# Kernel optimization log

Measured on AMD Instinct MI355X. Metric: run time of the kernel, lower is better.

## Reference

```python
import jax, jax.numpy as jnp
import numpy as np

B, C, CO, N = 2, 32, 32, 64
MODES, LMAX, RBINS = 16, 2, 16
HALF = MODES // 2
NL = (LMAX + 1) ** 2  # 9 real spherical harmonics up to l=2
M = MODES ** 3
HID = 16  # round(CO * 0.5)


def _build_basis():
    # frequencies of the kept FNO corner modes along each axis
    f = np.concatenate([np.arange(HALF), np.arange(-HALF, 0)]).astype(np.float32)
    kx, ky, kz = np.meshgrid(f, f, f, indexing='ij')
    kx, ky, kz = kx.ravel(), ky.ravel(), kz.ravel()
    r = np.sqrt(kx ** 2 + ky ** 2 + kz ** 2)
    nzm = (r > 0).astype(np.float32)
    inv = np.where(r > 0, 1.0 / np.maximum(r, 1e-9), 0.0)
    ux, uy, uz = kx * inv, ky * inv, kz * inv
    # real spherical harmonics l=0,1,2 (cartesian form); all l>0 vanish at DC
    Y = np.stack([
        0.282095 * np.ones_like(r),
        0.488603 * uy, 0.488603 * uz, 0.488603 * ux,
        1.092548 * ux * uy, 1.092548 * uy * uz,
        0.315392 * (3.0 * uz ** 2 - nzm),
        1.092548 * ux * uz, 0.546274 * (ux ** 2 - uy ** 2)], axis=0)  # [NL, M]
    shell = np.minimum((r / (r.max() + 1e-6) * RBINS).astype(np.int64), RBINS - 1)
    cnt = np.bincount(shell, minlength=RBINS).astype(np.float32)
    w = 1.0 / np.sqrt(np.maximum(cnt, 1.0))
    mask = (shell[None, :] == np.arange(RBINS)[:, None]).astype(np.float32) * w[:, None]  # [RBINS, M]
    return (mask[:, None, :] * Y[None]).reshape(RBINS * NL, M).astype(np.float32)

BASIS = jnp.asarray(_build_basis())  # [K=144, M=4096], fixed projection basis
IDX = jnp.asarray(np.concatenate([np.arange(HALF), np.arange(N - HALF, N)]))  # kept mode indices


def cgelu(z):
    return jax.nn.gelu(z.real) + 1j * jax.nn.gelu(z.imag)


def setup_inputs() -> dict:
    key = jax.random.key(0)
    ks = jax.random.split(key, 17)
    rn = lambda k, s: jax.random.normal(k, s, dtype=jnp.float32)
    return {
        'x': rn(ks[0], (B, C, N, N, N)),
        'w_fno_r': rn(ks[1], (CO, C)) * 0.1, 'w_fno_i': rn(ks[2], (CO, C)) * 0.1,
        'b_fno_r': rn(ks[3], (CO,)) * 0.1, 'b_fno_i': rn(ks[4], (CO,)) * 0.1,
        'w_gate_r': rn(ks[5], (CO,)), 'w_gate_i': rn(ks[6], (CO,)),
        'w_spec_r': rn(ks[7], (RBINS, NL, C, CO)) * 0.1, 'w_spec_i': rn(ks[8], (RBINS, NL, C, CO)) * 0.1,
        'mlp_w1_r': rn(ks[9], (HID, CO)) * 0.1, 'mlp_w1_i': rn(ks[10], (HID, CO)) * 0.1,
        'mlp_b1_r': rn(ks[11], (HID,)) * 0.1, 'mlp_b1_i': rn(ks[12], (HID,)) * 0.1,
        'mlp_w2_r': rn(ks[13], (CO, HID)) * 0.1, 'mlp_w2_i': rn(ks[14], (CO, HID)) * 0.1,
        'mlp_b2_r': rn(ks[15], (CO,)) * 0.1, 'mlp_b2_i': rn(ks[16], (CO,)) * 0.1,
    }


def reference(x, w_fno_r, w_fno_i, b_fno_r, b_fno_i, w_gate_r, w_gate_i,
              w_spec_r, w_spec_i, mlp_w1_r, mlp_w1_i, mlp_b1_r, mlp_b1_i,
              mlp_w2_r, mlp_w2_i, mlp_b2_r, mlp_b2_i):
    cx = lambda r, i: (r + 1j * i).astype(jnp.complex64)
    xc = x.astype(jnp.complex64)
    w_fno, b_fno = cx(w_fno_r, w_fno_i), cx(b_fno_r, b_fno_i)
    w_gate = cx(w_gate_r, w_gate_i)
    w_spec = cx(w_spec_r, w_spec_i)
    w1, b1 = cx(mlp_w1_r, mlp_w1_i), cx(mlp_b1_r, mlp_b1_i)
    w2, b2 = cx(mlp_w2_r, mlp_w2_i), cx(mlp_b2_r, mlp_b2_i)

    # skip paths: complex 1x1-conv ('linear') and complex soft-gating
    skip_fno = jnp.einsum('oc,bcxyz->boxyz', w_fno, xc) + b_fno[None, :, None, None, None]
    skip_mlp = xc * w_gate[None, :, None, None, None]

    # Harmonic layer: FFT -> slice kept modes -> harmonic/radial projection
    # -> complex spectral conv -> inverse projection -> scatter -> iFFT
    xf = jnp.fft.fftn(xc, axes=(-3, -2, -1))
    xs = xf[:, :, IDX[:, None, None], IDX[None, :, None], IDX[None, None, :]].reshape(B, C, M)
    coeffs = jnp.einsum('bcm,km->bck', xs, BASIS).reshape(B, C, RBINS, NL)
    coeffs = jnp.einsum('bisl,slio->bosl', coeffs, w_spec)
    xs2 = jnp.einsum('bck,km->bcm', coeffs.reshape(B, CO, RBINS * NL), BASIS)
    full = jnp.zeros((B, CO, N, N, N), jnp.complex64).at[
        :, :, IDX[:, None, None], IDX[None, :, None], IDX[None, None, :]
    ].set(xs2.reshape(B, CO, MODES, MODES, MODES))
    x_fno = jnp.fft.ifftn(full, axes=(-3, -2, -1))

    x1 = x_fno + skip_fno  # n_layers=1 -> no activation here
    h = cgelu(jnp.einsum('hc,bcxyz->bhxyz', w1, x1) + b1[None, :, None, None, None])
    y = jnp.einsum('oh,bhxyz->boxyz', w2, h) + b2[None, :, None, None, None]
    return (y + skip_mlp).real
```

## Files before the change

kernel.cpp:

```cpp
#include <hip/hip_runtime.h>
#include <hip/hip_bf16.h>

#define PI2 6.283185307179586f

typedef __attribute__((ext_vector_type(8))) short short8;
typedef __attribute__((ext_vector_type(4))) float f32x4;

static const size_t O_Y      = 0;
static const size_t O_W1RT   = 36864;
static const size_t O_W1IT   = 37376;
static const size_t O_W1XR   = 37888;
static const size_t O_W1XI   = 38400;
static const size_t O_B1PR   = 38912;
static const size_t O_B1PI   = 38928;
static const size_t O_WSH    = 38944;
static const size_t O_SHELL  = 38960;
static const size_t O_ORDER  = 43056;
static const size_t O_SSTART = 47152;
static const size_t O_COEF   = 47232;
static const size_t O_COEF2  = 65664;
static const size_t O_XS     = 84096;
static const size_t O_XS2    = 608384;
static const size_t O_T2     = 1132672;
static const size_t O_T1     = 3229824;

static __device__ __forceinline__ float geluf(float v) {
  float u = 0.7978845608028654f * (v + 0.044715f * v * v * v);
  float a = fabsf(u);
  float e = __expf(-2.0f * a);
  float th = (1.0f - e) / (1.0f + e);
  th = copysignf(th, u);
  return 0.5f * v * (1.0f + th);
}

static __device__ __forceinline__ unsigned int f2bfbits(float f) {
  unsigned int u = __float_as_uint(f);
  u += 0x7fffu + ((u >> 16) & 1u);
  return u >> 16;
}

static __device__ __forceinline__ unsigned int pk2(float a, float b) {
  return f2bfbits(a) | (f2bfbits(b) << 16);
}

__global__ __launch_bounds__(256) void k0_init(
    const float* __restrict__ wfr, const float* __restrict__ wfi,
    const float* __restrict__ bfr, const float* __restrict__ bfi,
    const float* __restrict__ w1r, const float* __restrict__ w1i,
    const float* __restrict__ b1r, const float* __restrict__ b1i,
    float* __restrict__ ws) {
  float* Y    = ws + O_Y;
  float* w1rt = ws + O_W1RT;  float* w1it = ws + O_W1IT;
  float* W1xr = ws + O_W1XR;  float* W1xi = ws + O_W1XI;
  float* b1pr = ws + O_B1PR;  float* b1pi = ws + O_B1PI;
  float* wsh  = ws + O_WSH;
  int* shellOf = (int*)(ws + O_SHELL);
  int* order   = (int*)(ws + O_ORDER);
  int* sstart  = (int*)(ws + O_SSTART);

  __shared__ int cnt[16], fill[16], st[17];
  int tid = threadIdx.x;
  if (tid < 16) { cnt[tid] = 0; fill[tid] = 0; }
  __syncthreads();
  for (int m = tid; m < 4096; m += 256) {
    int ix = m >> 8, iy = (m >> 4) & 15, iz = m & 15;
    float kx = (float)(ix < 8 ? ix : ix - 16);
    float ky = (float)(iy < 8 ? iy : iy - 16);
    float kz = (float)(iz < 8 ? iz : iz - 16);
    float r2 = kx*kx + ky*ky + kz*kz;
    float r  = sqrtf(r2);
    float nzm = r2 > 0.f ? 1.f : 0.f;
    float inv = r2 > 0.f ? 1.0f / fmaxf(r, 1e-9f) : 0.f;
    float ux = kx*inv, uy = ky*inv, uz = kz*inv;
    Y[0*4096+m] = 0.282095f;
    Y[1*4096+m] = 0.488603f * uy;
    Y[2*4096+m] = 0.488603f * uz;
    Y[3*4096+m] = 0.488603f * ux;
    Y[4*4096+m] = 1.092548f * ux*uy;
    Y[5*4096+m] = 1.092548f * uy*uz;
    Y[6*4096+m] = 0.315392f * (3.0f*uz*uz - nzm);
    Y[7*4096+m] = 1.092548f * ux*uz;
    Y[8*4096+m] = 0.546274f * (ux*ux - uy*uy);
    float rmax = sqrtf(192.0f);
    float t = r / (rmax + 1e-6f) * 16.0f;
    int sh = (int)t; sh = sh > 15 ? 15 : sh;
    shellOf[m] = sh;
    atomicAdd(&cnt[sh], 1);
  }
  __syncthreads();
  if (tid == 0) { int a = 0; for (int s = 0; s < 16; ++s) { st[s] = a; a += cnt[s]; } st[16] = a; }
  __syncthreads();
  if (tid < 16) wsh[tid] = 1.0f / sqrtf(fmaxf((float)cnt[tid], 1.0f));
  if (tid < 17) sstart[tid] = st[tid];
  for (int m = tid; m < 4096; m += 256) {
    int sh = shellOf[m];
    int p = atomicAdd(&fill[sh], 1);
    order[st[sh] + p] = m;
  }
  for (int e = tid; e < 512; e += 256) {
    int j = e >> 5, c = e & 31;
    float ar = 0.f, ai = 0.f;
    for (int o = 0; o < 32; ++o) {
      float wr_ = w1r[j*32+o], wi_ = w1i[j*32+o];
      float fr  = wfr[o*32+c], fi_ = wfi[o*32+c];
      ar += wr_*fr - wi_*fi_;
      ai += wr_*fi_ + wi_*fr;
    }
    W1xr[c*16+j] = ar;  W1xi[c*16+j] = ai;
    w1rt[c*16+j] = w1r[j*32+c];
    w1it[c*16+j] = w1i[j*32+c];
  }
  if (tid < 16) {
    int j = tid;
    float ar = b1r[j], ai = b1i[j];
    for (int o = 0; o < 32; ++o) {
      ar += w1r[j*32+o]*bfr[o] - w1i[j*32+o]*bfi[o];
      ai += w1r[j*32+o]*bfi[o] + w1i[j*32+o]*bfr[o];
    }
    b1pr[j] = ar; b1pi[j] = ai;
  }
}

__global__ __launch_bounds__(256) void k12_fwd(const float* __restrict__ x, float* __restrict__ T2) {
  __shared__ __align__(16) float zS[4096];
  __shared__ float2 slab[64*17];
  __shared__ float2 tw[16*17];
  float* zP = zS;  float* zQ = zS + 1024;  float* zB = zS + 2048;  float* zD = zS + 3072;
  float* ysum = zS;
  int blk = blockIdx.x;
  const float* src = x + (size_t)blk * 4096;
  int tid = threadIdx.x;

  {
    int y = tid >> 2, zt = tid & 3;
    const float4* s4 = (const float4*)(src + y*64);
    float4 u0 = s4[zt];
    float4 u1 = s4[zt + 4];
    float4 u2 = s4[zt + 8];
    float4 u3 = s4[zt + 12];
    const float* p0 = (const float*)&u0; const float* p1 = (const float*)&u1;
    const float* p2 = (const float*)&u2; const float* p3 = (const float*)&u3;
    int base = 4*zt*64 + y;
    #pragma unroll
    for (int e = 0; e < 4; ++e) {
      float a = p0[e] + p2[e], c = p1[e] + p3[e];
      float bb = p0[e] - p2[e], d = p1[e] - p3[e];
      zP[base + e*64] = a + c;
      zQ[base + e*64] = a - c;
      zB[base + e*64] = bb;
      zD[base + e*64] = d;
    }
  }
  {
    int k = tid >> 4, i2 = tid & 15;
    float f = (float)(k < 8 ? k : k - 16);
    float ang = -PI2 * f * (float)i2 / 64.0f;
    float sw, cw; __sincosf(ang, &sw, &cw);
    tw[k*17 + i2] = make_float2(cw, sw);
  }
  __syncthreads();

  {
    int kz = tid & 15, yq = tid >> 4;
    int j = kz & 3;
    const float2* twp = tw + kz*17;
    float arr[4] = {0.f,0.f,0.f,0.f}, aii[4] = {0.f,0.f,0.f,0.f};
    if ((j & 1) == 0) {
      const float* plane = (j == 0) ? zP : zQ;
      #pragma unroll
      for (int z0 = 0; z0 < 16; ++z0) {
        float2 w = twp[z0];
        float4 s = *(const float4*)&plane[z0*64 + 4*yq];
        arr[0] += s.x*w.x; aii[0] += s.x*w.y;
        arr[1] += s.y*w.x; aii[1] += s.y*w.y;
        arr[2] += s.z*w.x; aii[2] += s.z*w.y;
        arr[3] += s.w*w.x; aii[3] += s.w*w.y;
      }
    } else {
      float dsg = (j == 1) ? -1.f : 1.f;
      #pragma unroll
      for (int z0 = 0; z0 < 16; ++z0) {
        float2 w = twp[z0];
        float4 b = *(const float4*)&zB[z0*64 + 4*yq];
        float4 d = *(const float4*)&zD[z0*64 + 4*yq];
        float swi = dsg * w.y, swr = dsg * w.x;
        arr[0] += b.x*w.x - d.x*swi;  aii[0] += b.x*w.y + d.x*swr;
        arr[1] += b.y*w.x - d.y*swi;  aii[1] += b.y*w.y + d.y*swr;
        arr[2] += b.z*w.x - d.z*swi;  aii[2] += b.z*w.y + d.z*swr;
        arr[3] += b.w*w.x - d.w*swi;  aii[3] += b.w*w.y + d.w*swr;
      }
    }
    int y0 = 4*yq;
    slab[(y0+0)*17 + kz] = make_float2(arr[0], aii[0]);
    slab[(y0+1)*17 + kz] = make_float2(arr[1], aii[1]);
    slab[(y0+2)*17 + kz] = make_float2(arr[2], aii[2]);
    slab[(y0+3)*17 + kz] = make_float2(arr[3], aii[3]);
  }
  __syncthreads();

  {
    int y0 = tid >> 4, kz = tid & 15;
    float2 u0 = slab[(y0     )*17 + kz];
    float2 u1 = slab[(y0 + 16)*17 + kz];
    float2 u2 = slab[(y0 + 32)*17 + kz];
    float2 u3 = slab[(y0 + 48)*17 + kz];
    float Ar = u0.x + u2.x, Ai = u0.y + u2.y;
    float Br = u0.x - u2.x, Bi = u0.y - u2.y;
    float Cr = u1.x + u3.x, Ci = u1.y + u3.y;
    float Dr = u1.x - u3.x, Di = u1.y - u3.y;
    float* yp = ysum + y0*162 + kz*10;
    yp[0] = Ar + Cr;  yp[1] = Ai + Ci;
    yp[2] = Br + Di;  yp[3] = Bi - Dr;
    yp[4] = Ar - Cr;  yp[5] = Ai - Ci;
    yp[6] = Br - Di;  yp[7] = Bi + Dr;
  }
  __syncthreads();

  {
    int kz = tid & 15, kyi = tid >> 4;
    const float* yp = ysum + kz*10 + (kyi & 3)*2;
    const float2* twp = tw + kyi*17;
    float ar = 0.f, ai = 0.f;
    #pragma unroll
    for (int y0 = 0; y0 < 16; ++y0) {
      float sr = yp[y0*162], si = yp[y0*162 + 1];
      float2 w = twp[y0];
      ar += sr*w.x - si*w.y;
      ai += sr*w.y + si*w.x;
    }
    *(float2*)&T2[(size_t)blk*512 + (kyi*16 + kz)*2] = make_float2(ar, ai);
  }
}

__global__ __launch_bounds__(256) void k3_dftx(const float* __restrict__ T2, float* __restrict__ xs) {
  __shared__ float slab[64*34];
  __shared__ float xsum[2592];
  __shared__ float2 twx[16*17];
  int blk = blockIdx.x;
  int bc = blk >> 4, ky = blk & 15;
  int tid = threadIdx.x;
  for (int i = tid; i < 2048; i += 256) {
    int xr = i >> 5, rem = i & 31;
    slab[xr*34 + rem] = T2[((size_t)(bc*64 + xr)*16 + ky)*32 + rem];
  }
  {
    int k = tid >> 4, i2 = tid & 15;
    float f = (float)(k < 8 ? k : k - 16);
    float ang = -PI2 * f * (float)i2 / 64.0f;
    float sw, cw; __sincosf(ang, &sw, &cw);
    twx[k*17 + i2] = make_float2(cw, sw);
  }
  __syncthreads();
  {
    int x0 = tid >> 4, kz = tid & 15;
    const float2* sp = (const float2*)slab;
    float2 u0 = sp[(x0     )*17 + kz];
    float2 u1 = sp[(x0 + 16)*17 + kz];
    float2 u2 = sp[(x0 + 32)*17 + kz];
    float2 u3 = sp[(x0 + 48)*17 + kz];
    float Ar = u0.x + u2.x, Ai = u0.y + u2.y;
    float Br = u0.x - u2.x, Bi = u0.y - u2.y;
    float Cr = u1.x + u3.x, Ci = u1.y + u3.y;
    float Dr = u1.x - u3.x, Di = u1.y - u3.y;
    float* yp = xsum + x0*162 + kz*10;
    yp[0] = Ar + Cr;  yp[1] = Ai + Ci;
    yp[2] = Br + Di;  yp[3] = Bi - Dr;
    yp[4] = Ar - Cr;  yp[5] = Ai - Ci;
    yp[6] = Br - Di;  yp[7] = Bi + Dr;
  }
  __syncthreads();
  {
    int kz = tid & 15, kxi = tid >> 4;
    const float* yp = xsum + kz*10 + (kxi & 3)*2;
    const float2* twp = twx + kxi*17;
    float ar = 0.f, ai = 0.f;
    #pragma unroll
    for (int x0 = 0; x0 < 16; ++x0) {
      float sr = yp[x0*162], si = yp[x0*162 + 1];
      float2 w = twp[x0];
      ar += sr*w.x - si*w.y;
      ai += sr*w.y + si*w.x;
    }
    *(float2*)&xs[(size_t)bc*8192 + (kxi*256 + ky*16 + kz)*2] = make_float2(ar, ai);
  }
}

__global__ __launch_bounds__(256) void k4_proj(const float* __restrict__ xs, const float* __restrict__ Y,
    const int* __restrict__ order, const int* __restrict__ sstart, const float* __restrict__ wsh,
    float* __restrict__ coeffs) {
  int blk = blockIdx.x; int bc = blk >> 4, s = blk & 15;
  int tid = threadIdx.x;
  int st = sstart[s], en = sstart[s+1];
  float ar[9], ai[9];
  #pragma unroll
  for (int l = 0; l < 9; ++l) { ar[l] = 0.f; ai[l] = 0.f; }
  for (int ii = st + tid; ii < en; ii += 256) {
    int m = order[ii];
    float2 v = *(const float2*)&xs[(size_t)bc*8192 + m*2];
    #pragma unroll
    for (int l = 0; l < 9; ++l) {
      float yv = Y[l*4096 + m];
      ar[l] += yv * v.x; ai[l] += yv * v.y;
    }
  }
  #pragma unroll
  for (int l = 0; l < 9; ++l) {
    #pragma unroll
    for (int d = 1; d < 64; d <<= 1) {
      ar[l] += __shfl_xor(ar[l], d, 64);
      ai[l] += __shfl_xor(ai[l], d, 64);
    }
  }
  __shared__ float wred[4][18];
  int wv = tid >> 6, lane = tid & 63;
  if (lane == 0) {
    #pragma unroll
    for (int l = 0; l < 9; ++l) { wred[wv][l] = ar[l]; wred[wv][9 + l] = ai[l]; }
  }
  __syncthreads();
  if (tid < 18) {
    float sum = wred[0][tid] + wred[1][tid] + wred[2][tid] + wred[3][tid];
    float w = wsh[s];
    int l = tid < 9 ? tid : tid - 9;
    int ri = tid < 9 ? 0 : 1;
    coeffs[((size_t)bc*144 + s*9 + l)*2 + ri] = w * sum;
  }
}

__global__ __launch_bounds__(64) void k5_spec(const float* __restrict__ coeffs,
    const float* __restrict__ wsr, const float* __restrict__ wsi, float* __restrict__ coeffs2) {
  int blk = blockIdx.x;
  int b = blk / 144, sl = blk % 144;
  int o = threadIdx.x;
  if (o >= 32) return;
  float ar = 0.f, ai = 0.f;
  for (int i = 0; i < 32; ++i) {
    float cr = coeffs[((size_t)(b*32 + i)*144 + sl)*2];
    float ci = coeffs[((size_t)(b*32 + i)*144 + sl)*2 + 1];
    float wr = wsr[(sl*32 + i)*32 + o];
    float wi = wsi[(sl*32 + i)*32 + o];
    ar += cr*wr - ci*wi;
    ai += cr*wi + ci*wr;
  }
  const float sc = 1.0f / 262144.0f;
  coeffs2[((size_t)(b*32 + o)*144 + sl)*2]     = ar * sc;
  coeffs2[((size_t)(b*32 + o)*144 + sl)*2 + 1] = ai * sc;
}

__global__ __launch_bounds__(256) void k7_unproj(const float* __restrict__ coeffs2, const float* __restrict__ Y,
    const int* __restrict__ shellOf, const float* __restrict__ wsh, float* __restrict__ xs2) {
  int bo = blockIdx.x >> 4;
  int m = ((blockIdx.x & 15) << 8) | threadIdx.x;
  __shared__ float c2[288];
  for (int i = threadIdx.x; i < 288; i += 256) c2[i] = coeffs2[(size_t)bo*288 + i];
  __syncthreads();
  int sh = shellOf[m];
  float w = wsh[sh];
  float ar = 0.f, ai = 0.f;
  #pragma unroll
  for (int l = 0; l < 9; ++l) {
    float yv = Y[l*4096 + m];
    ar += yv * c2[(sh*9 + l)*2];
    ai += yv * c2[(sh*9 + l)*2 + 1];
  }
  xs2[(size_t)bo*8192 + m*2]     = w * ar;
  xs2[(size_t)bo*8192 + m*2 + 1] = w * ai;
}

__global__ __launch_bounds__(256) void k8_invx(const float* __restrict__ xs2, float* __restrict__ U1) {
  __shared__ float slab[512];
  int blk = blockIdx.x;
  int bo = blk >> 4, ky = blk & 15;
  int tid = threadIdx.x;
  for (int i = tid; i < 512; i += 256) {
    int kx = i >> 5, rem = i & 31;
    slab[i] = xs2[(size_t)bo*8192 + kx*512 + ky*32 + rem];
  }
  __syncthreads();
  int kz = tid & 15, grp = tid >> 4;
  float ang = PI2 * (float)grp / 64.0f;
  float sw, cw; __sincosf(ang, &sw, &cw);
  float tr = 1.f, ti = 0.f;
  float sjr[4] = {0.f,0.f,0.f,0.f}, sji[4] = {0.f,0.f,0.f,0.f};
  #pragma unroll
  for (int kx = 0; kx < 16; ++kx) {
    if (kx == 8) ti = -ti;
    float2 v = *(const float2*)&slab[(kx*16 + kz)*2];
    sjr[kx & 3] += v.x*tr - v.y*ti;
    sji[kx & 3] += v.x*ti + v.y*tr;
    float nt = tr*cw - ti*sw; ti = tr*sw + ti*cw; tr = nt;
  }
  float Ar = sjr[0]+sjr[2], Ai = sji[0]+sji[2];
  float Br = sjr[0]-sjr[2], Bi = sji[0]-sji[2];
  float Cr = sjr[1]+sjr[3], Ci = sji[1]+sji[3];
  float Dr = sjr[1]-sjr[3], Di = sji[1]-sji[3];
  *(float2*)&U1[((size_t)(bo*64 + grp     )*16 + ky)*32 + kz*2] = make_float2(Ar+Cr, Ai+Ci);
  *(float2*)&U1[((size_t)(bo*64 + grp + 16)*16 + ky)*32 + kz*2] = make_float2(Br-Di, Bi+Dr);
  *(float2*)&U1[((size_t)(bo*64 + grp + 32)*16 + ky)*32 + kz*2] = make_float2(Ar-Cr, Ai-Ci);
  *(float2*)&U1[((size_t)(bo*64 + grp + 48)*16 + ky)*32 + kz*2] = make_float2(Br+Di, Bi-Dr);
}

__global__ __launch_bounds__(256) void k9_invy(const float* __restrict__ U1, float* __restrict__ U2) {
  __shared__ float slab[512];
  int blk = blockIdx.x;
  int tid = threadIdx.x;
  const float* src = U1 + (size_t)blk * 512;
  for (int i = tid; i < 512; i += 256) slab[i] = src[i];
  __syncthreads();
  int kz = tid & 15, grp = tid >> 4;
  float ang = PI2 * (float)grp / 64.0f;
  float sw, cw; __sincosf(ang, &sw, &cw);
  float tr = 1.f, ti = 0.f;
  float sjr[4] = {0.f,0.f,0.f,0.f}, sji[4] = {0.f,0.f,0.f,0.f};
  #pragma unroll
  for (int ky = 0; ky < 16; ++ky) {
    if (ky == 8) ti = -ti;
    float2 v = *(const float2*)&slab[(ky*16 + kz)*2];
    sjr[ky & 3] += v.x*tr - v.y*ti;
    sji[ky & 3] += v.x*ti + v.y*tr;
    float nt = tr*cw - ti*sw; ti = tr*sw + ti*cw; tr = nt;
  }
  float Ar = sjr[0]+sjr[2], Ai = sji[0]+sji[2];
  float Br = sjr[0]-sjr[2], Bi = sji[0]-sji[2];
  float Cr = sjr[1]+sjr[3], Ci = sji[1]+sji[3];
  float Dr = sjr[1]-sjr[3], Di = sji[1]-sji[3];
  float* dst = U2 + (size_t)blk * 2048;
  *(float2*)&dst[((grp     )*16 + kz)*2] = make_float2(Ar+Cr, Ai+Ci);
  *(float2*)&dst[((grp + 16)*16 + kz)*2] = make_float2(Br-Di, Bi+Dr);
  *(float2*)&dst[((grp + 32)*16 + kz)*2] = make_float2(Ar-Cr, Ai-Ci);
  *(float2*)&dst[((grp + 48)*16 + kz)*2] = make_float2(Br+Di, Bi-Dr);
}

__global__ __launch_bounds__(256) void k10_final(
    const float* __restrict__ x, const float* __restrict__ U2,
    const float* __restrict__ ws,
    const float* __restrict__ w2r, const float* __restrict__ w2i,
    const float* __restrict__ b2r, const float* __restrict__ wgr,
    float* __restrict__ out) {
  const float* w1rt = ws + O_W1RT;  const float* w1it = ws + O_W1IT;
  const float* W1xr = ws + O_W1XR;  const float* W1xi = ws + O_W1XI;
  const float* b1pr = ws + O_B1PR;  const float* b1pi = ws + O_B1PI;

  __shared__ unsigned int xfT[128*33];
  __shared__ __hip_bfloat16 xlT[128*34];
  __shared__ f32x4 hpW4[272];
  unsigned int* hpW = (unsigned int*)hpW4;
  unsigned int* Bt  = (unsigned int*)hpW4;

  int tid = threadIdx.x;
  int blk = blockIdx.x;
  int yb = blk & 31, bx = blk >> 5;
  int b = bx >> 6, xr = bx & 63;
  int y0 = yb * 2;

  int lane = tid & 63, wv = tid >> 6;
  int p = lane & 15, q = lane >> 4;

  union U8 { short8 v; unsigned int u[4]; };

  U8 fAr, fAi;
  {
    int z = wv*16 + p;
    float arj[8], aij[8];
    #pragma unroll
    for (int j = 0; j < 8; ++j) {
      int k = 8*q + j;
      int kz = k & 15;
      float f = (float)(kz < 8 ? kz : kz - 16);
      float s, c; __sincosf(PI2 * f * (float)z / 64.0f, &s, &c);
      arj[j] = (k < 16) ? c : -s;
      aij[j] = (k < 16) ? s : c;
    }
    #pragma unroll
    for (int s2 = 0; s2 < 4; ++s2) {
      fAr.u[s2] = pk2(arj[2*s2], arj[2*s2+1]);
      fAi.u[s2] = pk2(aij[2*s2], aij[2*s2+1]);
    }
  }

  for (int i = tid; i < 1024; i += 256) {
    int ya = i >> 9, c = (i >> 4) & 31, zq = i & 15;
    const float4 v = *(const float4*)&x[(size_t)(b*32 + c)*262144 + (size_t)xr*4096
                                        + (size_t)(y0 + ya)*64 + 4*zq];
    int rb = ((ya << 6) + 4*zq)*34 + c;
    xlT[rb]       = __float2bfloat16(v.x);
    xlT[rb + 34]  = __float2bfloat16(v.y);
    xlT[rb + 68]  = __float2bfloat16(v.z);
    xlT[rb + 102] = __float2bfloat16(v.w);
  }
  {
    int ya = tid >> 7, o = (tid >> 2) & 31, t4 = tid & 3;
    const float4* g4 = (const float4*)(U2 + ((size_t)((b*32 + o)*64 + xr))*2048
                                       + (size_t)(y0 + ya)*32 + 8*t4);
    float4 ga = g4[0], gb = g4[1];
    unsigned int* bp = Bt + (ya*32 + o)*17;
    bp[2*t4]         = pk2(ga.x, ga.z);
    bp[2*t4 + 1]     = pk2(gb.x, gb.z);
    bp[8 + 2*t4]     = pk2(ga.y, ga.w);
    bp[8 + 2*t4 + 1] = pk2(gb.y, gb.w);
  }
  __syncthreads();

  {
    f32x4 zac = {0.f, 0.f, 0.f, 0.f};
    #pragma unroll
    for (int ya = 0; ya < 2; ++ya) {
      #pragma unroll
      for (int ot = 0; ot < 2; ++ot) {
        U8 fB;
        uint4 bv = *(const uint4*)(Bt + (ya*32 + ot*16 + p)*17 + 4*q);
        fB.u[0] = bv.x; fB.u[1] = bv.y; fB.u[2] = bv.z; fB.u[3] = bv.w;
        f32x4 Dr = __builtin_amdgcn_mfma_f32_16x16x32_bf16(fAr.v, fB.v, zac, 0, 0, 0);
        f32x4 Di = __builtin_amdgcn_mfma_f32_16x16x32_bf16(fAi.v, fB.v, zac, 0, 0, 0);
        int rowb = ya*64 + wv*16 + 4*q;
        #pragma unroll
        for (int r = 0; r < 4; ++r)
          xfT[(rowb + r)*33 + ot*16 + p] = pk2(Dr[r], Di[r]);
      }
    }
  }
  __syncthreads();

  {
    int wb = wv * 272;

    U8 fW1r, fW1i, fW1iN, fW1xr, fW1xi, fW2[2];
    #pragma unroll
    for (int s = 0; s < 4; ++s) {
      int c0 = 8*q + 2*s, c1 = c0 + 1;
      fW1r.u[s]  = pk2(w1rt[c0*16 + p], w1rt[c1*16 + p]);
      fW1i.u[s]  = pk2(w1it[c0*16 + p], w1it[c1*16 + p]);
      fW1iN.u[s] = fW1i.u[s] ^ 0x80008000u;
      fW1xr.u[s] = pk2(W1xr[c0*16 + p], W1xr[c1*16 + p]);
      fW1xi.u[s] = pk2(W1xi[c0*16 + p], W1xi[c1*16 + p]);
    }
    #pragma unroll
    for (int mt = 0; mt < 2; ++mt) {
      int o = mt*16 + p;
      #pragma unroll
      for (int s = 0; s < 4; ++s) {
        int k0 = 8*q + 2*s;
        float a  = (k0   < 16) ? w2r[o*16 + k0]      : -w2i[o*16 + k0 - 16];
        float bb = (k0+1 < 16) ? w2r[o*16 + k0 + 1]  : -w2i[o*16 + k0 - 15];
        fW2[mt].u[s] = pk2(a, bb);
      }
    }
    float4 b1r4 = *(const float4*)(b1pr + 4*q);
    float4 b1i4 = *(const float4*)(b1pi + 4*q);
    float b2a[2][4], wga[2][4];
    #pragma unroll
    for (int mt = 0; mt < 2; ++mt) {
      float4 t0 = *(const float4*)(b2r + mt*16 + 4*q);
      float4 t1 = *(const float4*)(wgr + mt*16 + 4*q);
      b2a[mt][0]=t0.x; b2a[mt][1]=t0.y; b2a[mt][2]=t0.z; b2a[mt][3]=t0.w;
      wga[mt][0]=t1.x; wga[mt][1]=t1.y; wga[mt][2]=t1.z; wga[mt][3]=t1.w;
    }
    float b1ra[4] = {b1r4.x, b1r4.y, b1r4.z, b1r4.w};
    float b1ia[4] = {b1i4.x, b1i4.y, b1i4.z, b1i4.w};

    f32x4 zacc = {0.f, 0.f, 0.f, 0.f};
    const unsigned int* xlW = (const unsigned int*)xlT;

    for (int tt = 0; tt < 2; ++tt) {
      int tile = wv*2 + tt;
      int ya = tile >> 2, zg = tile & 3;
      int row = ya*64 + zg*16 + p;

      unsigned int w8[8];
      #pragma unroll
      for (int jj = 0; jj < 8; ++jj) w8[jj] = xfT[row*33 + 8*q + jj];
      U8 FR, FI, XV;
      #pragma unroll
      for (int s = 0; s < 4; ++s) {
        FR.u[s] = __builtin_amdgcn_perm(w8[2*s+1], w8[2*s], 0x05040100u);
        FI.u[s] = __builtin_amdgcn_perm(w8[2*s+1], w8[2*s], 0x07060302u);
        XV.u[s] = xlW[row*17 + 4*q + s];
      }

      f32x4 accR = zacc, accI = zacc;
      accR = __builtin_amdgcn_mfma_f32_16x16x32_bf16(fW1r.v,  FR.v, accR, 0, 0, 0);
      accR = __builtin_amdgcn_mfma_f32_16x16x32_bf16(fW1iN.v, FI.v, accR, 0, 0, 0);
      accR = __builtin_amdgcn_mfma_f32_16x16x32_bf16(fW1xr.v, XV.v, accR, 0, 0, 0);
      accI = __builtin_amdgcn_mfma_f32_16x16x32_bf16(fW1r.v,  FI.v, accI, 0, 0, 0);
      accI = __builtin_amdgcn_mfma_f32_16x16x32_bf16(fW1i.v,  FR.v, accI, 0, 0, 0);
      accI = __builtin_amdgcn_mfma_f32_16x16x32_bf16(fW1xi.v, XV.v, accI, 0, 0, 0);

      float hr_[4], hi_[4];
      #pragma unroll
      for (int r = 0; r < 4; ++r) {
        hr_[r] = geluf(accR[r] + b1ra[r]);
        hi_[r] = geluf(accI[r] + b1ia[r]);
      }
      hpW[wb + 17*p + 2*q]     = pk2(hr_[0], hr_[1]);
      hpW[wb + 17*p + 2*q + 1] = pk2(hr_[2], hr_[3]);
      hpW[wb + 17*p + 8 + 2*q]     = pk2(hi_[0], hi_[1]);
      hpW[wb + 17*p + 8 + 2*q + 1] = pk2(hi_[2], hi_[3]);

      U8 FH;
      #pragma unroll
      for (int s = 0; s < 4; ++s) FH.u[s] = hpW[wb + 17*p + 4*q + s];

      #pragma unroll
      for (int mt = 0; mt < 2; ++mt) {
        f32x4 accO = __builtin_amdgcn_mfma_f32_16x16x32_bf16(fW2[mt].v, FH.v, zacc, 0, 0, 0);
        #pragma unroll
        for (int r = 0; r < 4; ++r) {
          int o = mt*16 + q*4 + r;
          int z = zg*16 + p;
          float xv = __bfloat162float(xlT[row*34 + o]);
          out[(size_t)(b*32 + o)*262144 + (size_t)xr*4096 + (size_t)(y0 + ya)*64 + z]
              = accO[r] + b2a[mt][r] + wga[mt][r]*xv;
        }
      }
    }
  }
}

extern "C" void kernel_launch(void* const* d_in, const int* in_sizes, int n_in,
                              void* d_out, int out_size, void* d_ws, size_t ws_size,
                              hipStream_t stream) {
  (void)in_sizes; (void)n_in; (void)out_size; (void)ws_size;
  const float* x   = (const float*)d_in[0];
  const float* wfr = (const float*)d_in[1];
  const float* wfi = (const float*)d_in[2];
  const float* bfr = (const float*)d_in[3];
  const float* bfi = (const float*)d_in[4];
  const float* wgr = (const float*)d_in[5];
  const float* wsr = (const float*)d_in[7];
  const float* wsi = (const float*)d_in[8];
  const float* w1r = (const float*)d_in[9];
  const float* w1i = (const float*)d_in[10];
  const float* b1r = (const float*)d_in[11];
  const float* b1i = (const float*)d_in[12];
  const float* w2r = (const float*)d_in[13];
  const float* w2i = (const float*)d_in[14];
  const float* b2r = (const float*)d_in[15];
  float* out = (float*)d_out;
  float* ws  = (float*)d_ws;

  float* T1      = ws + O_T1;
  float* T2      = ws + O_T2;
  float* xs      = ws + O_XS;
  float* xs2     = ws + O_XS2;
  float* coeffs  = ws + O_COEF;
  float* coeffs2 = ws + O_COEF2;
  float* Y       = ws + O_Y;
  int* shellOf   = (int*)(ws + O_SHELL);
  int* order     = (int*)(ws + O_ORDER);
  int* sstart    = (int*)(ws + O_SSTART);
  float* wsh     = ws + O_WSH;

  hipLaunchKernelGGL(k0_init,  dim3(1),    dim3(256), 0, stream, wfr, wfi, bfr, bfi, w1r, w1i, b1r, b1i, ws);
  hipLaunchKernelGGL(k12_fwd,  dim3(4096), dim3(256), 0, stream, x, T2);
  hipLaunchKernelGGL(k3_dftx,  dim3(1024), dim3(256), 0, stream, T2, xs);
  hipLaunchKernelGGL(k4_proj,  dim3(1024), dim3(256), 0, stream, xs, Y, order, sstart, wsh, coeffs);
  hipLaunchKernelGGL(k5_spec,  dim3(288),  dim3(64),  0, stream, coeffs, wsr, wsi, coeffs2);
  hipLaunchKernelGGL(k7_unproj,dim3(1024), dim3(256), 0, stream, coeffs2, Y, shellOf, wsh, xs2);
  hipLaunchKernelGGL(k8_invx,  dim3(1024), dim3(256), 0, stream, xs2, T2);
  hipLaunchKernelGGL(k9_invy,  dim3(4096), dim3(256), 0, stream, T2, T1);
  hipLaunchKernelGGL(k10_final,dim3(4096), dim3(256), 0, stream, x, T1, ws, w2r, w2i, b2r, wgr, out);
}
```

Measured before the change: 265.2 us.

## Fuse spectral conv, unprojection and inverse x-DFT; use bf16 MFMA for inverse y-DFT

Merges the spectral-weight contraction, the inverse harmonic projection and the inverse x-axis DFT into one kernel. Each block now recomputes the 144 spectral coefficients it needs for its (b,o) pair, using a transposed copy of the spectral weights built by a new prep kernel, so the coeffs2 and xs2 round trips through global memory go away. The inverse y-DFT is rewritten as a pair of 16x16x32 bf16 MFMA matmuls with twiddle factors computed in registers, replacing the scalar twiddle-recurrence loop. In exchange, the spectral contraction is repeated 16 times per (b,o) and the y-DFT drops to bf16 precision.

```diff
diff --git a/kernel.cpp b/kernel.cpp
--- a/kernel.cpp
+++ b/kernel.cpp
@@ -18,9 +18,8 @@
 static const size_t O_ORDER  = 43056;
 static const size_t O_SSTART = 47152;
 static const size_t O_COEF   = 47232;
-static const size_t O_COEF2  = 65664;
 static const size_t O_XS     = 84096;
-static const size_t O_XS2    = 608384;
+static const size_t O_WST    = 608384;
 static const size_t O_T2     = 1132672;
 static const size_t O_T1     = 3229824;
 
@@ -121,6 +120,17 @@
   }
 }
 
+__global__ __launch_bounds__(256) void k0b_wst(const float* __restrict__ wsr,
+    const float* __restrict__ wsi, float* __restrict__ ws) {
+  float* wst = ws + O_WST;
+  int o = blockIdx.x;
+  for (int e = threadIdx.x; e < 4608; e += 256) {
+    int i = e / 144, sl = e - i*144;
+    wst[(size_t)o*9216 + i*288 + sl*2]     = wsr[(sl*32 + i)*32 + o];
+    wst[(size_t)o*9216 + i*288 + sl*2 + 1] = wsi[(sl*32 + i)*32 + o];
+  }
+}
+
 __global__ __launch_bounds__(256) void k12_fwd(const float* __restrict__ x, float* __restrict__ T2) {
   __shared__ __align__(16) float zS[4096];
   __shared__ float2 slab[64*17];
@@ -327,56 +337,54 @@
   }
 }
 
-__global__ __launch_bounds__(64) void k5_spec(const float* __restrict__ coeffs,
-    const float* __restrict__ wsr, const float* __restrict__ wsi, float* __restrict__ coeffs2) {
-  int blk = blockIdx.x;
-  int b = blk / 144, sl = blk % 144;
-  int o = threadIdx.x;
-  if (o >= 32) return;
-  float ar = 0.f, ai = 0.f;
-  for (int i = 0; i < 32; ++i) {
-    float cr = coeffs[((size_t)(b*32 + i)*144 + sl)*2];
-    float ci = coeffs[((size_t)(b*32 + i)*144 + sl)*2 + 1];
-    float wr = wsr[(sl*32 + i)*32 + o];
-    float wi = wsi[(sl*32 + i)*32 + o];
-    ar += cr*wr - ci*wi;
-    ai += cr*wi + ci*wr;
-  }
-  const float sc = 1.0f / 262144.0f;
-  coeffs2[((size_t)(b*32 + o)*144 + sl)*2]     = ar * sc;
-  coeffs2[((size_t)(b*32 + o)*144 + sl)*2 + 1] = ai * sc;
-}
-
-__global__ __launch_bounds__(256) void k7_unproj(const float* __restrict__ coeffs2, const float* __restrict__ Y,
-    const int* __restrict__ shellOf, const float* __restrict__ wsh, float* __restrict__ xs2) {
-  int bo = blockIdx.x >> 4;
-  int m = ((blockIdx.x & 15) << 8) | threadIdx.x;
+__global__ __launch_bounds__(256) void k857(const float* __restrict__ coeffs,
+    const float* __restrict__ ws, float* __restrict__ U1) {
+  const float* wst = ws + O_WST;
+  const float* Y   = ws + O_Y;
+  const int* shellOf = (const int*)(ws + O_SHELL);
+  const float* wsh = ws + O_WSH;
   __shared__ float c2[288];
-  for (int i = threadIdx.x; i < 288; i += 256) c2[i] = coeffs2[(size_t)bo*288 + i];
-  __syncthreads();
-  int sh = shellOf[m];
-  float w = wsh[sh];
-  float ar = 0.f, ai = 0.f;
-  #pragma unroll
-  for (int l = 0; l < 9; ++l) {
-    float yv = Y[l*4096 + m];
-    ar += yv * c2[(sh*9 + l)*2];
-    ai += yv * c2[(sh*9 + l)*2 + 1];
-  }
-  xs2[(size_t)bo*8192 + m*2]     = w * ar;
-  xs2[(size_t)bo*8192 + m*2 + 1] = w * ai;
-}
-
-__global__ __launch_bounds__(256) void k8_invx(const float* __restrict__ xs2, float* __restrict__ U1) {
   __shared__ float slab[512];
   int blk = blockIdx.x;
   int bo = blk >> 4, ky = blk & 15;
+  int b = bo >> 5, o = bo & 31;
   int tid = threadIdx.x;
-  for (int i = tid; i < 512; i += 256) {
-    int kx = i >> 5, rem = i & 31;
-    slab[i] = xs2[(size_t)bo*8192 + kx*512 + ky*32 + rem];
-  }
-  __syncthreads();
+
+  if (tid < 144) {
+    int sl = tid;
+    const float* cp = coeffs + ((size_t)b*4608 + sl)*2;
+    const float* wp = wst + (size_t)o*9216 + sl*2;
+    float ar = 0.f, ai = 0.f;
+    #pragma unroll 4
+    for (int i = 0; i < 32; ++i) {
+      float cr = cp[i*288], ci = cp[i*288 + 1];
+      float wr = wp[i*288], wi = wp[i*288 + 1];
+      ar += cr*wr - ci*wi;
+      ai += cr*wi + ci*wr;
+    }
+    const float sc = 1.0f / 262144.0f;
+    c2[sl*2]     = ar * sc;
+    c2[sl*2 + 1] = ai * sc;
+  }
+  __syncthreads();
+
+  {
+    int kxi = tid >> 4, kz = tid & 15;
+    int m = kxi*256 + ky*16 + kz;
+    int sh = shellOf[m];
+    float w = wsh[sh];
+    float ar = 0.f, ai = 0.f;
+    #pragma unroll
+    for (int l = 0; l < 9; ++l) {
+      float yv = Y[l*4096 + m];
+      ar += yv * c2[(sh*9 + l)*2];
+      ai += yv * c2[(sh*9 + l)*2 + 1];
+    }
+    slab[tid*2]     = w * ar;
+    slab[tid*2 + 1] = w * ai;
+  }
+  __syncthreads();
+
   int kz = tid & 15, grp = tid >> 4;
   float ang = PI2 * (float)grp / 64.0f;
   float sw, cw; __sincosf(ang, &sw, &cw);
@@ -401,34 +409,64 @@
 }
 
 __global__ __launch_bounds__(256) void k9_invy(const float* __restrict__ U1, float* __restrict__ U2) {
-  __shared__ float slab[512];
+  __shared__ unsigned int Bt[16*17];
   int blk = blockIdx.x;
   int tid = threadIdx.x;
-  const float* src = U1 + (size_t)blk * 512;
-  for (int i = tid; i < 512; i += 256) slab[i] = src[i];
-  __syncthreads();
-  int kz = tid & 15, grp = tid >> 4;
-  float ang = PI2 * (float)grp / 64.0f;
-  float sw, cw; __sincosf(ang, &sw, &cw);
-  float tr = 1.f, ti = 0.f;
-  float sjr[4] = {0.f,0.f,0.f,0.f}, sji[4] = {0.f,0.f,0.f,0.f};
-  #pragma unroll
-  for (int ky = 0; ky < 16; ++ky) {
-    if (ky == 8) ti = -ti;
-    float2 v = *(const float2*)&slab[(ky*16 + kz)*2];
-    sjr[ky & 3] += v.x*tr - v.y*ti;
-    sji[ky & 3] += v.x*ti + v.y*tr;
-    float nt = tr*cw - ti*sw; ti = tr*sw + ti*cw; tr = nt;
-  }
-  float Ar = sjr[0]+sjr[2], Ai = sji[0]+sji[2];
-  float Br = sjr[0]-sjr[2], Bi = sji[0]-sji[2];
-  float Cr = sjr[1]+sjr[3], Ci = sji[1]+sji[3];
-  float Dr = sjr[1]-sjr[3], Di = sji[1]-sji[3];
-  float* dst = U2 + (size_t)blk * 2048;
-  *(float2*)&dst[((grp     )*16 + kz)*2] = make_float2(Ar+Cr, Ai+Ci);
-  *(float2*)&dst[((grp + 16)*16 + kz)*2] = make_float2(Br-Di, Bi+Dr);
-  *(float2*)&dst[((grp + 32)*16 + kz)*2] = make_float2(Ar-Cr, Ai-Ci);
-  *(float2*)&dst[((grp + 48)*16 + kz)*2] = make_float2(Br+Di, Bi-Dr);
+  int lane = tid & 63, wv = tid >> 6;
+  int p = lane & 15, q = lane >> 4;
+
+  union U8 { short8 v; unsigned int u[4]; };
+
+  U8 fAr, fAi;
+  {
+    int y = wv*16 + p;
+    float arj[8], aij[8];
+    #pragma unroll
+    for (int j = 0; j < 8; ++j) {
+      int k = 8*q + j;
+      int ky = k & 15;
+      float f = (float)(ky < 8 ? ky : ky - 16);
+      float s, c; __sincosf(PI2 * f * (float)y / 64.0f, &s, &c);
+      arj[j] = (k < 16) ? c : -s;
+      aij[j] = (k < 16) ? s : c;
+    }
+    #pragma unroll
+    for (int s2 = 0; s2 < 4; ++s2) {
+      fAr.u[s2] = pk2(arj[2*s2], arj[2*s2+1]);
+      fAi.u[s2] = pk2(aij[2*s2], aij[2*s2+1]);
+    }
+  }
+
+  {
+    int kz = tid >> 4, w = tid & 15;
+    const float* u = U1 + (size_t)blk * 512;
+    if (w < 8) {
+      float a = u[(2*w    )*32 + kz*2];
+      float b = u[(2*w + 1)*32 + kz*2];
+      Bt[kz*17 + w] = pk2(a, b);
+    } else {
+      int w2 = w - 8;
+      float a = u[(2*w2    )*32 + kz*2 + 1];
+      float b = u[(2*w2 + 1)*32 + kz*2 + 1];
+      Bt[kz*17 + w] = pk2(a, b);
+    }
+  }
+  __syncthreads();
+
+  {
+    U8 fB;
+    uint4 bv = *(const uint4*)(Bt + p*17 + 4*q);
+    fB.u[0] = bv.x; fB.u[1] = bv.y; fB.u[2] = bv.z; fB.u[3] = bv.w;
+    f32x4 zac = {0.f, 0.f, 0.f, 0.f};
+    f32x4 Dr = __builtin_amdgcn_mfma_f32_16x16x32_bf16(fAr.v, fB.v, zac, 0, 0, 0);
+    f32x4 Di = __builtin_amdgcn_mfma_f32_16x16x32_bf16(fAi.v, fB.v, zac, 0, 0, 0);
+    float2* dst = (float2*)(U2 + (size_t)blk * 2048);
+    #pragma unroll
+    for (int r = 0; r < 4; ++r) {
+      int y = wv*16 + 4*q + r;
+      dst[y*16 + p] = make_float2(Dr[r], Di[r]);
+    }
+  }
 }
 
 __global__ __launch_bounds__(256) void k10_final(
@@ -641,22 +679,18 @@
   float* T1      = ws + O_T1;
   float* T2      = ws + O_T2;
   float* xs      = ws + O_XS;
-  float* xs2     = ws + O_XS2;
   float* coeffs  = ws + O_COEF;
-  float* coeffs2 = ws + O_COEF2;
   float* Y       = ws + O_Y;
-  int* shellOf   = (int*)(ws + O_SHELL);
   int* order     = (int*)(ws + O_ORDER);
   int* sstart    = (int*)(ws + O_SSTART);
   float* wsh     = ws + O_WSH;
 
   hipLaunchKernelGGL(k0_init,  dim3(1),    dim3(256), 0, stream, wfr, wfi, bfr, bfi, w1r, w1i, b1r, b1i, ws);
+  hipLaunchKernelGGL(k0b_wst,  dim3(32),   dim3(256), 0, stream, wsr, wsi, ws);
   hipLaunchKernelGGL(k12_fwd,  dim3(4096), dim3(256), 0, stream, x, T2);
   hipLaunchKernelGGL(k3_dftx,  dim3(1024), dim3(256), 0, stream, T2, xs);
   hipLaunchKernelGGL(k4_proj,  dim3(1024), dim3(256), 0, stream, xs, Y, order, sstart, wsh, coeffs);
-  hipLaunchKernelGGL(k5_spec,  dim3(288),  dim3(64),  0, stream, coeffs, wsr, wsi, coeffs2);
-  hipLaunchKernelGGL(k7_unproj,dim3(1024), dim3(256), 0, stream, coeffs2, Y, shellOf, wsh, xs2);
-  hipLaunchKernelGGL(k8_invx,  dim3(1024), dim3(256), 0, stream, xs2, T2);
+  hipLaunchKernelGGL(k857,     dim3(1024), dim3(256), 0, stream, coeffs, ws, T2);
   hipLaunchKernelGGL(k9_invy,  dim3(4096), dim3(256), 0, stream, T2, T1);
   hipLaunchKernelGGL(k10_final,dim3(4096), dim3(256), 0, stream, x, T1, ws, w2r, w2i, b2r, wgr, out);
 }
```

Result: slower. 273.0 us (+2.9%).

## Fuse spectral mixing, inverse projection and inverse x-DFT into one kernel

Applied to the files above, without the earlier changes.

Merges the per-shell complex channel mixing (k5), the harmonic unprojection (k7) and the inverse x-axis DFT (k8) into a single kernel. Each block now recomputes the 144 spectral coefficients it needs for its (b,o) from coeffs and a pre-transposed weight array, builds its slab in shared memory, and runs the inverse DFT on it. This removes two launches and the coeffs2/xs2 global round trips. A new per-call kernel transposes the spectral weights so the loads are laid out per output channel. The cost is 16x redundant recomputation of the mixing per (b,o), since every ky block repeats it, plus one extra small launch.

```diff
diff --git a/kernel.cpp b/kernel.cpp
--- a/kernel.cpp
+++ b/kernel.cpp
@@ -18,9 +18,8 @@
 static const size_t O_ORDER  = 43056;
 static const size_t O_SSTART = 47152;
 static const size_t O_COEF   = 47232;
-static const size_t O_COEF2  = 65664;
 static const size_t O_XS     = 84096;
-static const size_t O_XS2    = 608384;
+static const size_t O_WST    = 608384;
 static const size_t O_T2     = 1132672;
 static const size_t O_T1     = 3229824;
 
@@ -121,6 +120,17 @@
   }
 }
 
+__global__ __launch_bounds__(256) void k0b_wst(const float* __restrict__ wsr,
+    const float* __restrict__ wsi, float* __restrict__ ws) {
+  float* wst = ws + O_WST;
+  int o = blockIdx.x;
+  for (int e = threadIdx.x; e < 4608; e += 256) {
+    int i = e / 144, sl = e - i*144;
+    wst[(size_t)o*9216 + i*288 + sl*2]     = wsr[(sl*32 + i)*32 + o];
+    wst[(size_t)o*9216 + i*288 + sl*2 + 1] = wsi[(sl*32 + i)*32 + o];
+  }
+}
+
 __global__ __launch_bounds__(256) void k12_fwd(const float* __restrict__ x, float* __restrict__ T2) {
   __shared__ __align__(16) float zS[4096];
   __shared__ float2 slab[64*17];
@@ -327,56 +337,54 @@
   }
 }
 
-__global__ __launch_bounds__(64) void k5_spec(const float* __restrict__ coeffs,
-    const float* __restrict__ wsr, const float* __restrict__ wsi, float* __restrict__ coeffs2) {
-  int blk = blockIdx.x;
-  int b = blk / 144, sl = blk % 144;
-  int o = threadIdx.x;
-  if (o >= 32) return;
-  float ar = 0.f, ai = 0.f;
-  for (int i = 0; i < 32; ++i) {
-    float cr = coeffs[((size_t)(b*32 + i)*144 + sl)*2];
-    float ci = coeffs[((size_t)(b*32 + i)*144 + sl)*2 + 1];
-    float wr = wsr[(sl*32 + i)*32 + o];
-    float wi = wsi[(sl*32 + i)*32 + o];
-    ar += cr*wr - ci*wi;
-    ai += cr*wi + ci*wr;
-  }
-  const float sc = 1.0f / 262144.0f;
-  coeffs2[((size_t)(b*32 + o)*144 + sl)*2]     = ar * sc;
-  coeffs2[((size_t)(b*32 + o)*144 + sl)*2 + 1] = ai * sc;
-}
-
-__global__ __launch_bounds__(256) void k7_unproj(const float* __restrict__ coeffs2, const float* __restrict__ Y,
-    const int* __restrict__ shellOf, const float* __restrict__ wsh, float* __restrict__ xs2) {
-  int bo = blockIdx.x >> 4;
-  int m = ((blockIdx.x & 15) << 8) | threadIdx.x;
+__global__ __launch_bounds__(256) void k857(const float* __restrict__ coeffs,
+    const float* __restrict__ ws, float* __restrict__ U1) {
+  const float* wst = ws + O_WST;
+  const float* Y   = ws + O_Y;
+  const int* shellOf = (const int*)(ws + O_SHELL);
+  const float* wsh = ws + O_WSH;
   __shared__ float c2[288];
-  for (int i = threadIdx.x; i < 288; i += 256) c2[i] = coeffs2[(size_t)bo*288 + i];
-  __syncthreads();
-  int sh = shellOf[m];
-  float w = wsh[sh];
-  float ar = 0.f, ai = 0.f;
-  #pragma unroll
-  for (int l = 0; l < 9; ++l) {
-    float yv = Y[l*4096 + m];
-    ar += yv * c2[(sh*9 + l)*2];
-    ai += yv * c2[(sh*9 + l)*2 + 1];
-  }
-  xs2[(size_t)bo*8192 + m*2]     = w * ar;
-  xs2[(size_t)bo*8192 + m*2 + 1] = w * ai;
-}
-
-__global__ __launch_bounds__(256) void k8_invx(const float* __restrict__ xs2, float* __restrict__ U1) {
   __shared__ float slab[512];
   int blk = blockIdx.x;
   int bo = blk >> 4, ky = blk & 15;
+  int b = bo >> 5, o = bo & 31;
   int tid = threadIdx.x;
-  for (int i = tid; i < 512; i += 256) {
-    int kx = i >> 5, rem = i & 31;
-    slab[i] = xs2[(size_t)bo*8192 + kx*512 + ky*32 + rem];
-  }
-  __syncthreads();
+
+  if (tid < 144) {
+    int sl = tid;
+    const float* cp = coeffs + ((size_t)b*4608 + sl)*2;
+    const float* wp = wst + (size_t)o*9216 + sl*2;
+    float ar = 0.f, ai = 0.f;
+    #pragma unroll 4
+    for (int i = 0; i < 32; ++i) {
+      float cr = cp[i*288], ci = cp[i*288 + 1];
+      float wr = wp[i*288], wi = wp[i*288 + 1];
+      ar += cr*wr - ci*wi;
+      ai += cr*wi + ci*wr;
+    }
+    const float sc = 1.0f / 262144.0f;
+    c2[sl*2]     = ar * sc;
+    c2[sl*2 + 1] = ai * sc;
+  }
+  __syncthreads();
+
+  {
+    int kxi = tid >> 4, kz = tid & 15;
+    int m = kxi*256 + ky*16 + kz;
+    int sh = shellOf[m];
+    float w = wsh[sh];
+    float ar = 0.f, ai = 0.f;
+    #pragma unroll
+    for (int l = 0; l < 9; ++l) {
+      float yv = Y[l*4096 + m];
+      ar += yv * c2[(sh*9 + l)*2];
+      ai += yv * c2[(sh*9 + l)*2 + 1];
+    }
+    slab[tid*2]     = w * ar;
+    slab[tid*2 + 1] = w * ai;
+  }
+  __syncthreads();
+
   int kz = tid & 15, grp = tid >> 4;
   float ang = PI2 * (float)grp / 64.0f;
   float sw, cw; __sincosf(ang, &sw, &cw);
@@ -641,22 +649,18 @@
   float* T1      = ws + O_T1;
   float* T2      = ws + O_T2;
   float* xs      = ws + O_XS;
-  float* xs2     = ws + O_XS2;
   float* coeffs  = ws + O_COEF;
-  float* coeffs2 = ws + O_COEF2;
   float* Y       = ws + O_Y;
-  int* shellOf   = (int*)(ws + O_SHELL);
   int* order     = (int*)(ws + O_ORDER);
   int* sstart    = (int*)(ws + O_SSTART);
   float* wsh     = ws + O_WSH;
 
   hipLaunchKernelGGL(k0_init,  dim3(1),    dim3(256), 0, stream, wfr, wfi, bfr, bfi, w1r, w1i, b1r, b1i, ws);
+  hipLaunchKernelGGL(k0b_wst,  dim3(32),   dim3(256), 0, stream, wsr, wsi, ws);
   hipLaunchKernelGGL(k12_fwd,  dim3(4096), dim3(256), 0, stream, x, T2);
   hipLaunchKernelGGL(k3_dftx,  dim3(1024), dim3(256), 0, stream, T2, xs);
   hipLaunchKernelGGL(k4_proj,  dim3(1024), dim3(256), 0, stream, xs, Y, order, sstart, wsh, coeffs);
-  hipLaunchKernelGGL(k5_spec,  dim3(288),  dim3(64),  0, stream, coeffs, wsr, wsi, coeffs2);
-  hipLaunchKernelGGL(k7_unproj,dim3(1024), dim3(256), 0, stream, coeffs2, Y, shellOf, wsh, xs2);
-  hipLaunchKernelGGL(k8_invx,  dim3(1024), dim3(256), 0, stream, xs2, T2);
+  hipLaunchKernelGGL(k857,     dim3(1024), dim3(256), 0, stream, coeffs, ws, T2);
   hipLaunchKernelGGL(k9_invy,  dim3(4096), dim3(256), 0, stream, T2, T1);
   hipLaunchKernelGGL(k10_final,dim3(4096), dim3(256), 0, stream, x, T1, ws, w2r, w2i, b2r, wgr, out);
 }
```

New measurement: 275.3 us. 1.04x slower.
